# Performance work log

Measured on AMD Instinct MI355X. Metric: run time of the kernel, lower is better.

Reference implementation:

```python
import jax, jax.numpy as jnp
import numpy as np

B, L, H, A = 2, 384, 256, 14  # batch, total residues (binder+target), hidden, atoms/residue


def setup_inputs() -> dict:
    key = jax.random.key(0)
    ks = jax.random.split(key, 8)
    s = 1.0 / np.sqrt(H)
    h = jax.random.normal(ks[0], (B, L, H), jnp.float32)          # encoder output
    X = jax.random.normal(ks[1], (B, L, A, 3), jnp.float32)       # coordinates
    mask = jnp.ones((B, L), jnp.int32)                             # residue validity mask
    Wx_w = jax.random.normal(ks[2], (H, H), jnp.float32) * s
    Wx_b = jnp.zeros((H,), jnp.float32)
    Ux_w = jax.random.normal(ks[3], (H, H), jnp.float32) * s
    Ux_b = jnp.zeros((H,), jnp.float32)
    Tx_w = jax.random.normal(ks[4], (A, H), jnp.float32) * s
    Tx_b = jnp.zeros((A,), jnp.float32)
    return dict(h=h, X=X, mask=mask, Wx_w=Wx_w, Wx_b=Wx_b,
                Ux_w=Ux_w, Ux_b=Ux_b, Tx_w=Tx_w, Tx_b=Tx_b)


def reference(h, X, mask, Wx_w, Wx_b, Ux_w, Ux_b, Tx_w, Tx_b):
    # One recurrent coordinate-update step of FADocker._forward.
    m = mask.astype(h.dtype)                                   # (B, L)
    hw = h @ Wx_w.T + Wx_b                                     # (B, L, H)  = W_x(h)
    hu = h @ Ux_w.T + Ux_b                                     # (B, L, H)  = U_x(h)
    mij = hw[:, :, None, :] + hu[:, None, :, :]                # (B, L, L, H)
    gate = jnp.einsum('bijh,ah->bija', jax.nn.relu(mij), Tx_w) + Tx_b  # (B, L, L, A) = T_x(mij)
    xij = (X[:, :, None] - X[:, None, :]) * gate[..., None]   # (B, L, L, A, 3)
    f = jnp.einsum('bijac,bj->biac', xij, m)                   # masked sum over j
    f = f / (1e-6 + m.sum(axis=1)[:, None, None, None])        # (B, L, A, 3)
    return X + jnp.clip(f, -20.0, 20.0)
```

## Files before the change

### kernel.cpp

```cpp
#include <hip/hip_runtime.h>
#include <hip/hip_fp16.h>

#define HDIM 256
#define LDIM 384
#define BDIM 2
#define ADIM 14

typedef __attribute__((ext_vector_type(8))) _Float16 f16x8;
typedef __attribute__((ext_vector_type(2))) _Float16 f16x2;
typedef __attribute__((ext_vector_type(4))) float f32x4;

static __device__ __forceinline__ unsigned pack_f16(float x, float y) {
    f16x2 t = {(_Float16)x, (_Float16)y};
    union { f16x2 v; unsigned u; } c; c.v = t;
    return c.u;
}

static __device__ __forceinline__ unsigned relu_add(unsigned a, unsigned b) {
    union { unsigned u; f16x2 v; } ua, ub, ur;
    ua.u = a; ub.u = b;
    const f16x2 z = {(_Float16)0.f, (_Float16)0.f};
    ur.v = __builtin_elementwise_max(ua.v + ub.v, z);
    return ur.u;
}

__global__ __launch_bounds__(256) void k_front(
    const float* __restrict__ h,
    const float* __restrict__ Wx_w, const float* __restrict__ Wx_b,
    const float* __restrict__ Ux_w, const float* __restrict__ Ux_b,
    const float* __restrict__ Tx_w,
    unsigned* __restrict__ hwP, unsigned* __restrict__ huP,
    unsigned* __restrict__ txP)
{
    const int tid = threadIdx.x;
    if (blockIdx.x == 384) {
        for (int idx = tid; idx < 16 * 128; idx += 256) {
            const int a = idx >> 7, k2 = idx & 127;
            unsigned v = 0;
            if (a < ADIM) {
                const float2 tw = *(const float2*)&Tx_w[a * HDIM + 2 * k2];
                v = pack_f16(tw.x, tw.y);
            }
            txP[idx] = v;
        }
        return;
    }
    const int w = tid >> 6, lane = tid & 63;
    const int n = lane & 15, quad = lane >> 4;
    const int g = blockIdx.x * 4 + w;
    const int ctile = g & 31;
    const int rtile = g >> 5;

    const int arow = (ctile & 15) * 16 + n;
    const float* __restrict__ Arow = (ctile < 16) ? &Wx_w[arow * HDIM]
                                                  : &Ux_w[arow * HDIM];
    const float* __restrict__ Brow = &h[(rtile * 16 + n) * HDIM];

    f32x4 acc = {0.f, 0.f, 0.f, 0.f};
    #pragma unroll
    for (int kc = 0; kc < 8; ++kc) {
        const int ko = kc * 32 + quad * 8;
        const float4 a0 = *(const float4*)&Arow[ko];
        const float4 a1 = *(const float4*)&Arow[ko + 4];
        const float4 b0 = *(const float4*)&Brow[ko];
        const float4 b1 = *(const float4*)&Brow[ko + 4];
        union { unsigned u[4]; f16x8 v; } af, bf;
        af.u[0] = pack_f16(a0.x, a0.y); af.u[1] = pack_f16(a0.z, a0.w);
        af.u[2] = pack_f16(a1.x, a1.y); af.u[3] = pack_f16(a1.z, a1.w);
        bf.u[0] = pack_f16(b0.x, b0.y); bf.u[1] = pack_f16(b0.z, b0.w);
        bf.u[2] = pack_f16(b1.x, b1.y); bf.u[3] = pack_f16(b1.z, b1.w);
        acc = __builtin_amdgcn_mfma_f32_16x16x32_f16(af.v, bf.v, acc, 0, 0, 0);
    }

    const int row = rtile * 16 + n;
    const int c0 = (ctile & 15) * 16 + quad * 4;
    const float4 bias = (ctile < 16) ? *(const float4*)&Wx_b[c0]
                                     : *(const float4*)&Ux_b[c0];
    uint2 pv;
    pv.x = pack_f16(acc[0] + bias.x, acc[1] + bias.y);
    pv.y = pack_f16(acc[2] + bias.z, acc[3] + bias.w);
    unsigned* __restrict__ dst = (ctile < 16) ? hwP : huP;
    *(uint2*)&dst[row * 128 + (ctile & 15) * 8 + quad * 2] = pv;
}

__global__ __launch_bounds__(384) void k_main(
    const unsigned* __restrict__ hwP, const unsigned* __restrict__ huP,
    const unsigned* __restrict__ txP,
    const float* __restrict__ X, const int* __restrict__ mask,
    const float* __restrict__ Tx_b,
    float* __restrict__ out)
{
    __shared__ float Xl[LDIM * 42];
    __shared__ float m_lds[LDIM];
    __shared__ float part2[2][24 * 16 * 4];
    __shared__ float part_m[24];

    const int i0 = blockIdx.x * 2, i1 = i0 + 1;
    const int b  = blockIdx.y;
    const int tid = threadIdx.x;
    const int w = tid >> 6, lane = tid & 63;
    const int n = lane & 15, quad = lane >> 4;

    {
        const float4* __restrict__ Xg4 = (const float4*)&X[b * (LDIM * 42)];
        float4* __restrict__ Xl4 = (float4*)Xl;
        for (int idx = tid; idx < LDIM * 42 / 4; idx += 384) Xl4[idx] = Xg4[idx];
        m_lds[tid] = (float)mask[b * LDIM + tid];
    }
    __syncthreads();

    const unsigned* __restrict__ hwr0 = &hwP[(b * LDIM + i0) * 128];
    const unsigned* __restrict__ hwr1 = &hwP[(b * LDIM + i1) * 128];
    const unsigned* __restrict__ hub  = &huP[b * LDIM * 128];
    const unsigned* __restrict__ txr  = &txP[n * 128];

    f32x4 acc0[4], acc1[4];
    #pragma unroll
    for (int t = 0; t < 4; ++t) {
        acc0[t] = (f32x4){0.f, 0.f, 0.f, 0.f};
        acc1[t] = (f32x4){0.f, 0.f, 0.f, 0.f};
    }

    #pragma unroll 2
    for (int kc = 0; kc < 8; ++kc) {
        const int ko = kc * 16 + quad * 4;
        const uint4 hwa = *(const uint4*)&hwr0[ko];
        const uint4 hwb = *(const uint4*)&hwr1[ko];
        const uint4 tx4 = *(const uint4*)&txr[ko];
        union { unsigned u[4]; f16x8 v; } bfrag;
        bfrag.u[0] = tx4.x; bfrag.u[1] = tx4.y;
        bfrag.u[2] = tx4.z; bfrag.u[3] = tx4.w;
        #pragma unroll
        for (int t = 0; t < 4; ++t) {
            const int j = (w * 4 + t) * 16 + n;
            const uint4 hu4 = *(const uint4*)&hub[j * 128 + ko];
            union { unsigned u[4]; f16x8 v; } af;
            af.u[0] = relu_add(hwa.x, hu4.x);
            af.u[1] = relu_add(hwa.y, hu4.y);
            af.u[2] = relu_add(hwa.z, hu4.z);
            af.u[3] = relu_add(hwa.w, hu4.w);
            acc0[t] = __builtin_amdgcn_mfma_f32_16x16x32_f16(af.v, bfrag.v, acc0[t], 0, 0, 0);
            af.u[0] = relu_add(hwb.x, hu4.x);
            af.u[1] = relu_add(hwb.y, hu4.y);
            af.u[2] = relu_add(hwb.z, hu4.z);
            af.u[3] = relu_add(hwb.w, hu4.w);
            acc1[t] = __builtin_amdgcn_mfma_f32_16x16x32_f16(af.v, bfrag.v, acc1[t], 0, 0, 0);
        }
    }

    float pm = 0.f;
    #pragma unroll
    for (int ii = 0; ii < 2; ++ii) {
        const f32x4* acc = ii ? acc1 : acc0;
        float s1 = 0.f, s2x = 0.f, s2y = 0.f, s2z = 0.f;
        if (n < ADIM) {
            const float txb = Tx_b[n];
            #pragma unroll
            for (int t = 0; t < 4; ++t) {
                #pragma unroll
                for (int r = 0; r < 4; ++r) {
                    const int jd = (w * 4 + t) * 16 + quad * 4 + r;
                    const float m = m_lds[jd];
                    const float g = acc[t][r] + txb;
                    const float mg = m * g;
                    const float* __restrict__ Xp = &Xl[jd * 42 + n * 3];
                    s1 += mg;
                    s2x = fmaf(mg, Xp[0], s2x);
                    s2y = fmaf(mg, Xp[1], s2y);
                    s2z = fmaf(mg, Xp[2], s2z);
                    if (ii == 0) pm += m;
                }
            }
        }
        f32x4 sv = {s2x, s2y, s2z, s1};
        *(f32x4*)&part2[ii][((w * 4 + quad) * 16 + n) * 4] = sv;
    }
    if (n == 0) part_m[w * 4 + quad] = pm;
    __syncthreads();

    int ii = -1, t42 = 0;
    if (tid < 42)                    { ii = 0; t42 = tid; }
    else if (tid >= 64 && tid < 106) { ii = 1; t42 = tid - 64; }
    if (ii >= 0) {
        const int a = t42 / 3, c = t42 % 3;
        const int i = ii ? i1 : i0;
        float S2 = 0.f, S1 = 0.f, msum = 0.f;
        #pragma unroll 4
        for (int g = 0; g < 24; ++g) {
            const float* __restrict__ p = &part2[ii][(g * 16 + a) * 4];
            S2 += p[c]; S1 += p[3]; msum += part_m[g];
        }
        const float denom = 1e-6f + msum;
        const float xi = Xl[i * 42 + t42];
        float f = (xi * S1 - S2) / denom;
        f = fminf(fmaxf(f, -20.f), 20.f);
        out[((b * LDIM + i) * ADIM + a) * 3 + c] = xi + f;
    }
}

extern "C" void kernel_launch(void* const* d_in, const int* in_sizes, int n_in,
                              void* d_out, int out_size, void* d_ws, size_t ws_size,
                              hipStream_t stream) {
    (void)in_sizes; (void)n_in; (void)out_size; (void)ws_size;
    const float* h    = (const float*)d_in[0];
    const float* X    = (const float*)d_in[1];
    const int*   mask = (const int*)  d_in[2];
    const float* Wx_w = (const float*)d_in[3];
    const float* Wx_b = (const float*)d_in[4];
    const float* Ux_w = (const float*)d_in[5];
    const float* Ux_b = (const float*)d_in[6];
    const float* Tx_w = (const float*)d_in[7];
    const float* Tx_b = (const float*)d_in[8];
    float* out = (float*)d_out;

    unsigned* hwP = (unsigned*)d_ws;
    unsigned* huP = hwP + BDIM * LDIM * (HDIM / 2);
    unsigned* txP = huP + BDIM * LDIM * (HDIM / 2);

    k_front<<<385, 256, 0, stream>>>(h, Wx_w, Wx_b, Ux_w, Ux_b, Tx_w, hwP, huP, txP);
    k_main<<<dim3(LDIM / 2, BDIM), 384, 0, stream>>>(hwP, huP, txP, X, mask, Tx_b, out);
}
```

Baseline: 101.4 us.

## Drop LDS staging of X and pre-packed Tx_w; read directly from global

Removes the per-block copy of the whole batch's coordinates (about 64KB) into shared memory and reads X straight from global/L2 during the reduction and epilogue. It also drops the extra k_front block that packed Tx_w to fp16, so k_main loads Tx_w floats and converts them inline. The aim is to cut the large redundant LDS fill per block and raise occupancy by freeing shared memory. The cost is scattered global loads of X in the epilogue and repeated fp32-to-fp16 conversion of the Tx_w fragments.

```diff
diff --git a/kernel.cpp b/kernel.cpp
--- a/kernel.cpp
+++ b/kernel.cpp
@@ -28,23 +28,9 @@
     const float* __restrict__ h,
     const float* __restrict__ Wx_w, const float* __restrict__ Wx_b,
     const float* __restrict__ Ux_w, const float* __restrict__ Ux_b,
-    const float* __restrict__ Tx_w,
-    unsigned* __restrict__ hwP, unsigned* __restrict__ huP,
-    unsigned* __restrict__ txP)
+    unsigned* __restrict__ hwP, unsigned* __restrict__ huP)
 {
     const int tid = threadIdx.x;
-    if (blockIdx.x == 384) {
-        for (int idx = tid; idx < 16 * 128; idx += 256) {
-            const int a = idx >> 7, k2 = idx & 127;
-            unsigned v = 0;
-            if (a < ADIM) {
-                const float2 tw = *(const float2*)&Tx_w[a * HDIM + 2 * k2];
-                v = pack_f16(tw.x, tw.y);
-            }
-            txP[idx] = v;
-        }
-        return;
-    }
     const int w = tid >> 6, lane = tid & 63;
     const int n = lane & 15, quad = lane >> 4;
     const int g = blockIdx.x * 4 + w;
@@ -85,12 +71,10 @@
 
 __global__ __launch_bounds__(384) void k_main(
     const unsigned* __restrict__ hwP, const unsigned* __restrict__ huP,
-    const unsigned* __restrict__ txP,
+    const float* __restrict__ Tx_w, const float* __restrict__ Tx_b,
     const float* __restrict__ X, const int* __restrict__ mask,
-    const float* __restrict__ Tx_b,
     float* __restrict__ out)
 {
-    __shared__ float Xl[LDIM * 42];
     __shared__ float m_lds[LDIM];
     __shared__ float part2[2][24 * 16 * 4];
     __shared__ float part_m[24];
@@ -101,18 +85,13 @@
     const int w = tid >> 6, lane = tid & 63;
     const int n = lane & 15, quad = lane >> 4;
 
-    {
-        const float4* __restrict__ Xg4 = (const float4*)&X[b * (LDIM * 42)];
-        float4* __restrict__ Xl4 = (float4*)Xl;
-        for (int idx = tid; idx < LDIM * 42 / 4; idx += 384) Xl4[idx] = Xg4[idx];
-        m_lds[tid] = (float)mask[b * LDIM + tid];
-    }
+    m_lds[tid] = (float)mask[b * LDIM + tid];
     __syncthreads();
 
     const unsigned* __restrict__ hwr0 = &hwP[(b * LDIM + i0) * 128];
     const unsigned* __restrict__ hwr1 = &hwP[(b * LDIM + i1) * 128];
     const unsigned* __restrict__ hub  = &huP[b * LDIM * 128];
-    const unsigned* __restrict__ txr  = &txP[n * 128];
+    const int nn = (n < ADIM) ? n : 0;
 
     f32x4 acc0[4], acc1[4];
     #pragma unroll
@@ -126,10 +105,11 @@
         const int ko = kc * 16 + quad * 4;
         const uint4 hwa = *(const uint4*)&hwr0[ko];
         const uint4 hwb = *(const uint4*)&hwr1[ko];
-        const uint4 tx4 = *(const uint4*)&txr[ko];
+        const float4 t0 = *(const float4*)&Tx_w[nn * HDIM + kc * 32 + quad * 8];
+        const float4 t1 = *(const float4*)&Tx_w[nn * HDIM + kc * 32 + quad * 8 + 4];
         union { unsigned u[4]; f16x8 v; } bfrag;
-        bfrag.u[0] = tx4.x; bfrag.u[1] = tx4.y;
-        bfrag.u[2] = tx4.z; bfrag.u[3] = tx4.w;
+        bfrag.u[0] = pack_f16(t0.x, t0.y); bfrag.u[1] = pack_f16(t0.z, t0.w);
+        bfrag.u[2] = pack_f16(t1.x, t1.y); bfrag.u[3] = pack_f16(t1.z, t1.w);
         #pragma unroll
         for (int t = 0; t < 4; ++t) {
             const int j = (w * 4 + t) * 16 + n;
@@ -163,7 +143,7 @@
                     const float m = m_lds[jd];
                     const float g = acc[t][r] + txb;
                     const float mg = m * g;
-                    const float* __restrict__ Xp = &Xl[jd * 42 + n * 3];
+                    const float* __restrict__ Xp = &X[((b * LDIM + jd) * ADIM + n) * 3];
                     s1 += mg;
                     s2x = fmaf(mg, Xp[0], s2x);
                     s2y = fmaf(mg, Xp[1], s2y);
@@ -191,10 +171,11 @@
             S2 += p[c]; S1 += p[3]; msum += part_m[g];
         }
         const float denom = 1e-6f + msum;
-        const float xi = Xl[i * 42 + t42];
+        const int idx = ((b * LDIM + i) * ADIM + a) * 3 + c;
+        const float xi = X[idx];
         float f = (xi * S1 - S2) / denom;
         f = fminf(fmaxf(f, -20.f), 20.f);
-        out[((b * LDIM + i) * ADIM + a) * 3 + c] = xi + f;
+        out[idx] = xi + f;
     }
 }
 
@@ -215,8 +196,7 @@
 
     unsigned* hwP = (unsigned*)d_ws;
     unsigned* huP = hwP + BDIM * LDIM * (HDIM / 2);
-    unsigned* txP = huP + BDIM * LDIM * (HDIM / 2);
-
-    k_front<<<385, 256, 0, stream>>>(h, Wx_w, Wx_b, Ux_w, Ux_b, Tx_w, hwP, huP, txP);
-    k_main<<<dim3(LDIM / 2, BDIM), 384, 0, stream>>>(hwP, huP, txP, X, mask, Tx_b, out);
-}
+
+    k_front<<<384, 256, 0, stream>>>(h, Wx_w, Wx_b, Ux_w, Ux_b, hwP, huP);
+    k_main<<<dim3(LDIM / 2, BDIM), 384, 0, stream>>>(hwP, huP, Tx_w, Tx_b, X, mask, out);
+}
```

Measured after the change: 100.5 us. About the same (-0.8%).
